# Kernel optimization log

Hardware: AMD Instinct MI355X
Metric: run time of the kernel (lower is better)

The kernel has to match this reference:

```python
import jax, jax.numpy as jnp
import numpy as np
import math

N = 20000          # nodes (residues)
E = 640000         # edges
CS = 384           # c_s
CZ = 128           # c_z
CH = 16            # c_hidden
H = 8              # no_heads
PQK = 8            # no_qk_points == no_v_points (forced equal, see notes)
FS = 128           # scalar channels in feat_irreps
PIN = 16           # vector channels in feat_irreps
HC = H * CH        # 128
HPQ = H * PQK * 3  # 192
CZ4 = CZ // 4      # 32
OUT_IN = HC + 3 * H + H + H * CZ4  # 416 actual concat width
INF = 100000.0
EPS = 1e-8


def setup_inputs() -> dict:
    key = jax.random.key(0)
    ks = jax.random.split(key, 16)
    w = lambda k, i, o: (jax.random.normal(k, (i, o), jnp.float32) / np.float32(np.sqrt(i)))
    frame_s = jax.random.normal(ks[0], (N, CS), jnp.float32)
    tfn_t = jax.random.normal(ks[1], (N, FS + 3 * PIN), jnp.float32)
    z = jax.random.normal(ks[2], (E, CZ), jnp.float32)
    edge_index = jax.random.randint(ks[3], (2, E), 0, N)
    mask = jnp.ones((N,), jnp.float32)
    # Rigid transforms: proper-ish rotations via QR, translations
    rot, _ = jnp.linalg.qr(jax.random.normal(ks[4], (N, 3, 3), jnp.float32))
    trans = jax.random.normal(ks[5], (N, 3), jnp.float32)
    return {
        "frame_s": frame_s, "tfn_t": tfn_t, "z": z,
        "edge_index": edge_index, "mask": mask,
        "rot": rot, "trans": trans,
        "Wq": w(ks[6], CS, HC), "bq": jnp.zeros((HC,), jnp.float32),
        "Wk_s": w(ks[7], FS, HC), "Wk_v": w(ks[8], PIN, PQK),
        "Wqp": w(ks[9], CS, HPQ), "bqp": jnp.zeros((HPQ,), jnp.float32),
        "Wb": w(ks[10], CZ, H), "bb": jnp.zeros((H,), jnp.float32),
        "Wdz": w(ks[11], CZ, CZ4), "bdz": jnp.zeros((CZ4,), jnp.float32),
        # ipa_point_weights_init_: softplus(hw) == 1  =>  hw = log(e - 1)
        "head_weights": jnp.full((H,), np.float32(np.log(np.e - 1.0))),
        "Wout": w(ks[12], OUT_IN, CS), "bout": jnp.zeros((CS,), jnp.float32),
    }


def _segment_softmax(a, seg, n):
    # pyg-style numerically stable segment softmax over edges grouped by seg
    m = jax.ops.segment_max(a, seg, num_segments=n)
    m = jnp.where(jnp.isfinite(m), m, 0.0)
    e = jnp.exp(a - m[seg])
    s = jax.ops.segment_sum(e, seg, num_segments=n)
    return e / (s[seg] + 1e-16)


def _forward(frame_s, tfn_t, z, mask, rot, trans,
             Wq, bq, Wk_s, Wk_v, Wqp, bqp, Wb, bb, Wdz, bdz,
             head_weights, Wout, bout, edge_index):
    n = frame_s.shape[0]
    src = edge_index[1]
    dst = edge_index[0]

    # scalar queries: [N,H,C]
    q = (frame_s @ Wq + bq).reshape(n, H, CH)

    # o3.Linear (feat_irreps -> k_irreps): scalars mix scalars, vectors mix vectors.
    # NOTE: original code uses linear_k for BOTH k and v (faithful bug), so v==k.
    scal = tfn_t[:, :FS]
    vecs = tfn_t[:, FS:].reshape(n, PIN, 3)
    k_scal = scal @ Wk_s                                   # [N, HC]
    k_vec = jnp.einsum('npx,pq->nqx', vecs, Wk_v)          # [N, PQK, 3]
    k = k_scal.reshape(n, H, CH)
    v = k
    k_tail = k_vec.reshape(n, PQK * 3)                     # [N, 24]
    # torch: split([3]*PQK) then stack(dim=-1) -> [N,3,PQK], then view [N,H,-1,3]
    k_pts = jnp.stack(jnp.split(k_tail, PQK, axis=-1), axis=-1)  # [N,3,PQK]
    k_pts = k_pts.reshape(n, H, -1, 3)                     # [N,H,1,3]
    v_pts = k_pts

    # query points, rigid-transformed: [N,H,PQK,3]
    q_pts = frame_s @ Wqp + bqp                            # [N, 3*H*PQK]
    q_pts = jnp.stack(jnp.split(q_pts, 3, axis=-1), axis=-1)  # [N, H*PQK, 3]
    q_pts = jnp.einsum('nij,npj->npi', rot, q_pts) + trans[:, None, :]
    q_pts = q_pts.reshape(n, H, PQK, 3)

    # scalar attention logits [E,H]
    a = jnp.einsum('ehc,ehc->eh', q[src], k[dst])
    a = a * np.float32(math.sqrt(1.0 / (3 * CH)))
    b = z @ Wb + bb                                        # [E,H]
    a = a + np.float32(math.sqrt(1.0 / 3)) * b

    # point attention: disp [E,H,PQK,3] (k_pts broadcasts over points)
    disp = q_pts[src] - k_pts[dst]
    pt_att = jnp.sum(disp * disp, axis=-1)                 # [E,H,PQK]
    hw = jax.nn.softplus(head_weights) * np.float32(math.sqrt(1.0 / (3 * (PQK * 9.0 / 2))))
    pt_att = -0.5 * jnp.sum(pt_att * hw[None, :, None], axis=-1)  # [E,H]

    edge_mask = INF * (mask[dst] * mask[src] - 1.0)        # [E]
    a = a + pt_att + edge_mask[:, None]

    a = _segment_softmax(a, src, n)                        # [E,H]

    # scalar output
    o = jax.ops.segment_sum(a[..., None] * v[dst], src, num_segments=n)  # [N,H,C]
    o = o.reshape(n, HC)

    # point output
    o_pt = jax.ops.segment_sum(a[:, :, None, None] * v_pts[dst], src, num_segments=n)  # [N,H,1,3]
    o_pt = jnp.einsum('nji,nhpj->nhpi', rot, o_pt - trans[:, None, None, :])  # invert_apply
    o_pt_norm = jnp.sqrt(jnp.sum(o_pt * o_pt, axis=-1) + EPS).reshape(n, H)
    o_pt = o_pt.reshape(n, -1, 3)                          # [N,H,3]

    # pair output
    pair_z = z @ Wdz + bdz                                 # [E,CZ4]
    o_pair = jax.ops.segment_sum(a[..., None] * pair_z[:, None, :], src, num_segments=n)  # [N,H,CZ4]
    o_pair = o_pair.reshape(n, H * CZ4)

    feats = jnp.concatenate(
        [o, o_pt[..., 0], o_pt[..., 1], o_pt[..., 2], o_pt_norm, o_pair], axis=-1)  # [N,416]
    return feats @ Wout + bout                             # [N, CS]


def reference(frame_s, tfn_t, z, edge_index, mask, rot, trans,
              Wq, bq, Wk_s, Wk_v, Wqp, bqp, Wb, bb, Wdz, bdz,
              head_weights, Wout, bout):
    return _forward(frame_s, tfn_t, z, mask, rot, trans,
                    Wq, bq, Wk_s, Wk_v, Wqp, bqp, Wb, bb, Wdz, bdz,
                    head_weights, Wout, bout, edge_index)
```

## Files before the change

### kernel.cpp

```cpp
#include <hip/hip_runtime.h>
#include <math.h>

typedef __attribute__((ext_vector_type(8))) short short8;
typedef __attribute__((ext_vector_type(4))) float f32x4;

static __device__ inline unsigned short f2bf(float f) {
    union { float f; unsigned u; } v; v.f = f;
    unsigned r = v.u + 0x7FFF + ((v.u >> 16) & 1);
    return (unsigned short)(r >> 16);
}

template<int WJ>
__device__ __forceinline__ void gemm_body(
    unsigned short* __restrict__ As, unsigned short* __restrict__ Bs,
    const float* __restrict__ A, int lda,
    const float* __restrict__ BT, int ldb,
    const float* __restrict__ bias,
    float* __restrict__ C, int ldc,
    int M, int N, int K, int bx, int by)
{
    constexpr int GBN = WJ * 32;
    const int t = threadIdx.x;
    const int wid = t >> 6, lane = t & 63;
    const int wm = (wid & 1) * 64;
    const int wn = (wid >> 1) * (WJ * 16);
    const int row16 = lane & 15, quad = lane >> 4;
    const int bm = bx * 128;
    const int bn = by * GBN;

    f32x4 acc[4][WJ];
    #pragma unroll
    for (int i = 0; i < 4; ++i)
        #pragma unroll
        for (int j = 0; j < WJ; ++j)
            #pragma unroll
            for (int r = 0; r < 4; ++r) acc[i][j][r] = 0.f;

    const int ktiles = (K + 63) >> 6;
    for (int kt = 0; kt < ktiles; ++kt) {
        const int k0 = kt << 6;
        #pragma unroll
        for (int it = 0; it < 8; ++it) {
            int f = it * 256 + t;
            int row = f >> 4, kq = (f & 15) << 2;
            float4 av = make_float4(0.f, 0.f, 0.f, 0.f);
            if (bm + row < M && k0 + kq < K)
                av = *(const float4*)(A + (size_t)(bm + row) * lda + k0 + kq);
            ushort4 uv;
            uv.x = f2bf(av.x); uv.y = f2bf(av.y); uv.z = f2bf(av.z); uv.w = f2bf(av.w);
            *(ushort4*)(&As[row * 72 + kq]) = uv;
        }
        #pragma unroll
        for (int it = 0; it < WJ * 2; ++it) {
            int f = it * 256 + t;
            int row = f >> 4, kq = (f & 15) << 2;
            float4 bv = make_float4(0.f, 0.f, 0.f, 0.f);
            if (bn + row < N && k0 + kq < K)
                bv = *(const float4*)(BT + (size_t)(bn + row) * ldb + k0 + kq);
            ushort4 uv;
            uv.x = f2bf(bv.x); uv.y = f2bf(bv.y); uv.z = f2bf(bv.z); uv.w = f2bf(bv.w);
            *(ushort4*)(&Bs[row * 72 + kq]) = uv;
        }
        __syncthreads();

        #pragma unroll
        for (int ks = 0; ks < 64; ks += 32) {
            short8 af[4], bfv[WJ];
            #pragma unroll
            for (int i = 0; i < 4; ++i)
                af[i] = *(const short8*)(&As[(wm + i * 16 + row16) * 72 + ks + quad * 8]);
            #pragma unroll
            for (int j = 0; j < WJ; ++j)
                bfv[j] = *(const short8*)(&Bs[(wn + j * 16 + row16) * 72 + ks + quad * 8]);
            #pragma unroll
            for (int i = 0; i < 4; ++i)
                #pragma unroll
                for (int j = 0; j < WJ; ++j)
                    acc[i][j] = __builtin_amdgcn_mfma_f32_16x16x32_bf16(af[i], bfv[j], acc[i][j], 0, 0, 0);
        }
        __syncthreads();
    }

    #pragma unroll
    for (int i = 0; i < 4; ++i)
        #pragma unroll
        for (int j = 0; j < WJ; ++j) {
            int col = bn + wn + j * 16 + row16;
            if (col >= N) continue;
            float bv = bias ? bias[col] : 0.f;
            #pragma unroll
            for (int r = 0; r < 4; ++r) {
                int row = bm + wm + i * 16 + quad * 4 + r;
                if (row < M) C[(size_t)row * ldc + col] = acc[i][j][r] + bv;
            }
        }
}

template<int WJ>
__global__ __launch_bounds__(256) void gemm_mfma(
    const float* __restrict__ A, int lda,
    const float* __restrict__ BT, int ldb,
    const float* __restrict__ bias,
    float* __restrict__ C, int ldc,
    int M, int N, int K)
{
    __shared__ unsigned short As[128 * 72];
    __shared__ unsigned short Bs[WJ * 32 * 72];
    gemm_body<WJ>(As, Bs, A, lda, BT, ldb, bias, C, ldc, M, N, K, blockIdx.x, blockIdx.y);
}

__device__ __forceinline__ void bpair_body(
    const float* __restrict__ z, const float* __restrict__ wcatT,
    const float* __restrict__ bcat, float* __restrict__ bpair, int E,
    int bb, int nbb)
{
    const int lane = threadIdx.x & 63;
    const int wid = threadIdx.x >> 6;
    const int row16 = lane & 15, quad = lane >> 4;

    short8 bfv[3][4];
    float bj[3];
    #pragma unroll
    for (int j = 0; j < 3; ++j) {
        int col = j * 16 + row16;
        bool cv = col < 40;
        bj[j] = cv ? bcat[col] : 0.f;
        #pragma unroll
        for (int ks = 0; ks < 4; ++ks) {
            float4 w0 = make_float4(0.f, 0.f, 0.f, 0.f);
            float4 w1 = make_float4(0.f, 0.f, 0.f, 0.f);
            if (cv) {
                const float* wp = wcatT + (size_t)col * 128 + ks * 32 + quad * 8;
                w0 = *(const float4*)(wp);
                w1 = *(const float4*)(wp + 4);
            }
            short8 f;
            f[0] = (short)f2bf(w0.x); f[1] = (short)f2bf(w0.y);
            f[2] = (short)f2bf(w0.z); f[3] = (short)f2bf(w0.w);
            f[4] = (short)f2bf(w1.x); f[5] = (short)f2bf(w1.y);
            f[6] = (short)f2bf(w1.z); f[7] = (short)f2bf(w1.w);
            bfv[j][ks] = f;
        }
    }

    const int nstrips = (E + 31) >> 5;
    const int gw = bb * 4 + wid;
    const int nw = nbb * 4;
    for (int st = gw; st < nstrips; st += nw) {
        const int r0 = st * 32;
        short8 af[2][4];
        #pragma unroll
        for (int i = 0; i < 2; ++i) {
            int row = r0 + i * 16 + row16;
            bool rv = row < E;
            const float* zp = z + (size_t)row * 128 + quad * 8;
            #pragma unroll
            for (int ks = 0; ks < 4; ++ks) {
                float4 a0 = make_float4(0.f, 0.f, 0.f, 0.f);
                float4 a1 = make_float4(0.f, 0.f, 0.f, 0.f);
                if (rv) {
                    a0 = *(const float4*)(zp + ks * 32);
                    a1 = *(const float4*)(zp + ks * 32 + 4);
                }
                short8 f;
                f[0] = (short)f2bf(a0.x); f[1] = (short)f2bf(a0.y);
                f[2] = (short)f2bf(a0.z); f[3] = (short)f2bf(a0.w);
                f[4] = (short)f2bf(a1.x); f[5] = (short)f2bf(a1.y);
                f[6] = (short)f2bf(a1.z); f[7] = (short)f2bf(a1.w);
                af[i][ks] = f;
            }
        }

        f32x4 acc[2][3];
        #pragma unroll
        for (int i = 0; i < 2; ++i)
            #pragma unroll
            for (int j = 0; j < 3; ++j)
                #pragma unroll
                for (int r = 0; r < 4; ++r) acc[i][j][r] = 0.f;

        #pragma unroll
        for (int ks = 0; ks < 4; ++ks)
            #pragma unroll
            for (int i = 0; i < 2; ++i)
                #pragma unroll
                for (int j = 0; j < 3; ++j)
                    acc[i][j] = __builtin_amdgcn_mfma_f32_16x16x32_bf16(af[i][ks], bfv[j][ks], acc[i][j], 0, 0, 0);

        #pragma unroll
        for (int i = 0; i < 2; ++i)
            #pragma unroll
            for (int j = 0; j < 3; ++j) {
                int col = j * 16 + row16;
                if (col >= 40) continue;
                #pragma unroll
                for (int r = 0; r < 4; ++r) {
                    int row = r0 + i * 16 + quad * 4 + r;
                    if (row < E) bpair[(size_t)row * 40 + col] = acc[i][j][r] + bj[j];
                }
            }
    }
}

__global__ __launch_bounds__(256) void mega_kernel(
    const float* __restrict__ z, const float* __restrict__ wcatT,
    const float* __restrict__ bcat, float* __restrict__ bpair, int E,
    const float* __restrict__ frame_s, const float* __restrict__ wqqpT,
    const float* __restrict__ bqqp, float* __restrict__ qqp, int n,
    const float* __restrict__ tfn, const float* __restrict__ wksT,
    float* __restrict__ kbuf,
    const float* __restrict__ Wkv, float* __restrict__ kpts,
    const int* __restrict__ srcA, const int* __restrict__ dstA,
    int* __restrict__ cur, int2* __restrict__ einfo,
    int nb_bp, int nb_qqp_x, int nb_qqp, int nb_k, int nb_kpts)
{
    __shared__ unsigned short As[128 * 72];
    __shared__ unsigned short Bs[128 * 72];
    int b = blockIdx.x;
    if (b < nb_bp) {
        bpair_body(z, wcatT, bcat, bpair, E, b, nb_bp);
        return;
    }
    b -= nb_bp;
    if (b < nb_qqp) {
        gemm_body<4>(As, Bs, frame_s, 384, wqqpT, 384, bqqp, qqp, 320, n, 320, 384,
                     b % nb_qqp_x, b / nb_qqp_x);
        return;
    }
    b -= nb_qqp;
    if (b < nb_k) {
        gemm_body<4>(As, Bs, tfn, 176, wksT, 128, nullptr, kbuf, 128, n, 128, 128, b, 0);
        return;
    }
    b -= nb_k;
    if (b < nb_kpts) {
        int t = b * 256 + threadIdx.x;
        if (t < n * 24) {
            int node = t / 24, f = t % 24;
            int a = f >> 3;
            int bb2 = f & 7;
            const float* vr = tfn + (size_t)node * 176 + 128;
            float s = 0.f;
            #pragma unroll
            for (int p = 0; p < 16; ++p) s += vr[p * 3 + a] * Wkv[p * 8 + bb2];
            kpts[t] = s;
        }
        return;
    }
    b -= nb_kpts;
    {
        int e = b * 256 + threadIdx.x;
        if (e < E) {
            int s = srcA[e];
            int pos = atomicAdd(&cur[s], 1);
            einfo[pos] = make_int2(e, dstA[e]);
        }
    }
}

__global__ void prep_count_kernel(
    const float* __restrict__ Wq, const float* __restrict__ bq,
    const float* __restrict__ Wqp, const float* __restrict__ bqp,
    const float* __restrict__ Wb, const float* __restrict__ bb,
    const float* __restrict__ Wdz, const float* __restrict__ bdz,
    const float* __restrict__ Wks, const float* __restrict__ Wout,
    float* __restrict__ wqqpT, float* __restrict__ bqqp,
    float* __restrict__ wcatT, float* __restrict__ bcat,
    float* __restrict__ wksT, float* __restrict__ woutT,
    const int* __restrict__ srcA, int* __restrict__ cnt, int E, int nb_cnt)
{
    int b = blockIdx.x;
    if (b < nb_cnt) {
        int e = b * 256 + threadIdx.x;
        if (e < E) atomicAdd(&cnt[srcA[e]], 1);
        return;
    }
    b -= nb_cnt;
    const float SC_QK = 0.14433756729740643f;
    const float SC_B  = 0.5773502691896258f;
    int gid = b * 256 + threadIdx.x;
    int stride = (gridDim.x - nb_cnt) * 256;
    for (int i = gid; i < 320 * 384; i += stride) {
        int o = i / 384, c = i % 384;
        wqqpT[i] = (o < 128) ? Wq[c * 128 + o] * SC_QK : Wqp[c * 192 + (o - 128)];
    }
    for (int i = gid; i < 320; i += stride) bqqp[i] = (i < 128) ? bq[i] * SC_QK : bqp[i - 128];
    for (int i = gid; i < 40 * 128; i += stride) {
        int o = i >> 7, c = i & 127;
        wcatT[i] = (o < 8) ? Wb[c * 8 + o] * SC_B : Wdz[c * 32 + (o - 8)];
    }
    for (int i = gid; i < 40; i += stride) bcat[i] = (i < 8) ? bb[i] * SC_B : bdz[i - 8];
    for (int i = gid; i < 128 * 128; i += stride) {
        int o = i >> 7, c = i & 127;
        wksT[i] = Wks[c * 128 + o];
    }
    for (int i = gid; i < 384 * 416; i += stride) {
        int o = i / 416, c = i % 416;
        woutT[i] = Wout[c * 384 + o];
    }
}

__global__ void scan_kernel(const int* __restrict__ cnt, int* __restrict__ off,
                            int* __restrict__ cur, int n)
{
    __shared__ int sums[1024];
    int t = threadIdx.x;
    int chunk = (n + 1023) >> 10;
    int begin = t * chunk;
    int local = 0;
    for (int j = 0; j < chunk; ++j) {
        int i = begin + j;
        if (i < n) local += cnt[i];
    }
    sums[t] = local;
    __syncthreads();
    for (int d = 1; d < 1024; d <<= 1) {
        int x = sums[t];
        int y = (t >= d) ? sums[t - d] : 0;
        __syncthreads();
        sums[t] = x + y;
        __syncthreads();
    }
    int run = sums[t] - local;
    for (int j = 0; j < chunk; ++j) {
        int i = begin + j;
        if (i < n) {
            off[i] = run;
            cur[i] = run;
            run += cnt[i];
        }
    }
}

__global__ __launch_bounds__(256) void attn_kernel(
    const int* __restrict__ off, const int* __restrict__ cnt,
    const int2* __restrict__ einfo,
    const float* __restrict__ qqp, const float* __restrict__ kbuf,
    const float* __restrict__ kpts,
    const float* __restrict__ bpair, const float* __restrict__ mask,
    const float* __restrict__ hwin,
    const float* __restrict__ rot, const float* __restrict__ trans,
    float* __restrict__ feats, int n)
{
    int wave = threadIdx.x >> 6;
    int lane = threadIdx.x & 63;
    int s = blockIdx.x * 4 + wave;
    if (s >= n) return;
    int es = lane >> 3;
    int h  = lane & 7;

    float qh[16];
    {
        const float* qp = qqp + (size_t)s * 320 + h * 16;
        #pragma unroll
        for (int c = 0; c < 16; ++c) qh[c] = qp[c];
    }
    const float* Rp = rot + (size_t)s * 9;
    const float* Tp = trans + (size_t)s * 3;
    float R0 = Rp[0], R1 = Rp[1], R2 = Rp[2];
    float R3 = Rp[3], R4 = Rp[4], R5 = Rp[5];
    float R6 = Rp[6], R7 = Rp[7], R8 = Rp[8];
    float T0 = Tp[0], T1 = Tp[1], T2 = Tp[2];
    float qpt[24];
    {
        const float* qr = qqp + (size_t)s * 320 + 128 + h * 8;
        #pragma unroll
        for (int p2 = 0; p2 < 8; ++p2) {
            float c0 = qr[p2], c1 = qr[64 + p2], c2 = qr[128 + p2];
            qpt[p2 * 3 + 0] = R0 * c0 + R1 * c1 + R2 * c2 + T0;
            qpt[p2 * 3 + 1] = R3 * c0 + R4 * c1 + R5 * c2 + T1;
            qpt[p2 * 3 + 2] = R6 * c0 + R7 * c1 + R8 * c2 + T2;
        }
    }
    float hwv = log1pf(__expf(hwin[h])) * 0.04811252243246882f;
    float mask_s = mask[s];
    int myoff = off[s], mycnt = cnt[s];

    float ssum = 0.f;
    float oacc[16];
    #pragma unroll
    for (int c = 0; c < 16; ++c) oacc[c] = 0.f;
    float optacc[3] = {0.f, 0.f, 0.f};
    float opacc[8][4];
    #pragma unroll
    for (int j = 0; j < 8; ++j)
        #pragma unroll
        for (int c = 0; c < 4; ++c) opacc[j][c] = 0.f;

    int nb = (mycnt + 7) >> 3;
    int2 ed = make_int2(0, 0);
    if (nb > 0) {
        int pos0 = (es < mycnt) ? myoff + es : (mycnt > 0 ? myoff : 0);
        ed = einfo[pos0];
    }
    for (int b = 0; b < nb; ++b) {
        int idx = b * 8 + es;
        bool valid = idx < mycnt;
        int e = ed.x, d = ed.y;
        int2 ned = ed;
        if (b + 1 < nb) {
            int nidx = idx + 8;
            int npos = (nidx < mycnt) ? myoff + nidx : myoff;
            ned = einfo[npos];
        }

        const float* kr = kbuf + (size_t)d * 128 + h * 16;
        float4 ka = *(const float4*)(kr + 0);
        float4 kb = *(const float4*)(kr + 4);
        float4 kc = *(const float4*)(kr + 8);
        float4 kd = *(const float4*)(kr + 12);

        const float* kp = kpts + (size_t)d * 24 + h * 3;
        float kp0 = kp[0], kp1 = kp[1], kp2 = kp[2];

        const float* bp = bpair + (size_t)e * 40;
        float bh = bp[h];
        float4 pair4 = *(const float4*)(bp + 8 + h * 4);

        float qk = qh[0] * ka.x + qh[1] * ka.y + qh[2] * ka.z + qh[3] * ka.w
                 + qh[4] * kb.x + qh[5] * kb.y + qh[6] * kb.z + qh[7] * kb.w
                 + qh[8] * kc.x + qh[9] * kc.y + qh[10] * kc.z + qh[11] * kc.w
                 + qh[12] * kd.x + qh[13] * kd.y + qh[14] * kd.z + qh[15] * kd.w;

        float pt = 0.f;
        #pragma unroll
        for (int pp = 0; pp < 8; ++pp) {
            float d0 = qpt[pp * 3 + 0] - kp0;
            float d1 = qpt[pp * 3 + 1] - kp1;
            float d2 = qpt[pp * 3 + 2] - kp2;
            pt += d0 * d0 + d1 * d1 + d2 * d2;
        }

        float md = mask[d];
        float logit = qk + bh - hwv * pt + 100000.0f * (mask_s * md - 1.0f);
        float w = valid ? __expf(logit) : 0.f;

        ssum += w;
        oacc[0] += w * ka.x; oacc[1] += w * ka.y; oacc[2] += w * ka.z; oacc[3] += w * ka.w;
        oacc[4] += w * kb.x; oacc[5] += w * kb.y; oacc[6] += w * kb.z; oacc[7] += w * kb.w;
        oacc[8] += w * kc.x; oacc[9] += w * kc.y; oacc[10] += w * kc.z; oacc[11] += w * kc.w;
        oacc[12] += w * kd.x; oacc[13] += w * kd.y; oacc[14] += w * kd.z; oacc[15] += w * kd.w;
        optacc[0] += w * kp0;
        optacc[1] += w * kp1;
        optacc[2] += w * kp2;

        #pragma unroll
        for (int jh = 0; jh < 8; ++jh) {
            float wj = __shfl(w, (es << 3) + jh);
            opacc[jh][0] += wj * pair4.x;
            opacc[jh][1] += wj * pair4.y;
            opacc[jh][2] += wj * pair4.z;
            opacc[jh][3] += wj * pair4.w;
        }
        ed = ned;
    }

    #pragma unroll
    for (int delta = 8; delta <= 32; delta <<= 1) {
        ssum += __shfl_xor(ssum, delta);
        #pragma unroll
        for (int c = 0; c < 16; ++c) oacc[c] += __shfl_xor(oacc[c], delta);
        #pragma unroll
        for (int i = 0; i < 3; ++i) optacc[i] += __shfl_xor(optacc[i], delta);
        #pragma unroll
        for (int j = 0; j < 8; ++j)
            #pragma unroll
            for (int c = 0; c < 4; ++c) opacc[j][c] += __shfl_xor(opacc[j][c], delta);
    }

    float invj[8];
    #pragma unroll
    for (int jh = 0; jh < 8; ++jh)
        invj[jh] = 1.f / (__shfl(ssum, jh) + 1e-16f);

    if (es == 0) {
        float inv = 1.f / (ssum + 1e-16f);
        float* f = feats + (size_t)s * 416;
        #pragma unroll
        for (int c = 0; c < 16; c += 4) {
            float4 v = make_float4(oacc[c] * inv, oacc[c + 1] * inv, oacc[c + 2] * inv, oacc[c + 3] * inv);
            *(float4*)(&f[h * 16 + c]) = v;
        }
        float v0 = optacc[0] * inv - T0;
        float v1 = optacc[1] * inv - T1;
        float v2 = optacc[2] * inv - T2;
        float r0 = R0 * v0 + R3 * v1 + R6 * v2;
        float r1 = R1 * v0 + R4 * v1 + R7 * v2;
        float r2 = R2 * v0 + R5 * v1 + R8 * v2;
        f[128 + h] = r0;
        f[136 + h] = r1;
        f[144 + h] = r2;
        f[152 + h] = sqrtf(r0 * r0 + r1 * r1 + r2 * r2 + 1e-8f);
        #pragma unroll
        for (int jh = 0; jh < 8; ++jh) {
            float4 v = make_float4(opacc[jh][0] * invj[jh], opacc[jh][1] * invj[jh],
                                   opacc[jh][2] * invj[jh], opacc[jh][3] * invj[jh]);
            *(float4*)(&f[160 + jh * 32 + h * 4]) = v;
        }
    }
}

extern "C" void kernel_launch(void* const* d_in, const int* in_sizes, int n_in,
                              void* d_out, int out_size, void* d_ws, size_t ws_size,
                              hipStream_t stream)
{
    const float* frame_s = (const float*)d_in[0];
    const float* tfn     = (const float*)d_in[1];
    const float* z       = (const float*)d_in[2];
    const int*   ei      = (const int*)d_in[3];
    const float* mask    = (const float*)d_in[4];
    const float* rot     = (const float*)d_in[5];
    const float* trans   = (const float*)d_in[6];
    const float* Wq      = (const float*)d_in[7];
    const float* bq      = (const float*)d_in[8];
    const float* Wks     = (const float*)d_in[9];
    const float* Wkv     = (const float*)d_in[10];
    const float* Wqp     = (const float*)d_in[11];
    const float* bqp     = (const float*)d_in[12];
    const float* Wb      = (const float*)d_in[13];
    const float* bb      = (const float*)d_in[14];
    const float* Wdz     = (const float*)d_in[15];
    const float* bdz     = (const float*)d_in[16];
    const float* hw      = (const float*)d_in[17];
    const float* Wout    = (const float*)d_in[18];
    const float* bout    = (const float*)d_in[19];
    float* out = (float*)d_out;

    int n = in_sizes[0] / 384;
    int E = in_sizes[3] / 2;
    const int* dstA = ei;
    const int* srcA = ei + E;

    float* ws = (float*)d_ws;
    size_t p = 0;
    auto alloc = [&](size_t elems) -> float* {
        float* r = ws + p;
        p += (elems + 15) & ~((size_t)15);
        return r;
    };
    float* qqpbuf = alloc((size_t)n * 320);
    float* kbuf   = alloc((size_t)n * 128);
    float* kpts   = alloc((size_t)n * 24);
    float* feats  = alloc((size_t)n * 416);
    float* bpair  = alloc((size_t)E * 40);
    float* wqqpT  = alloc(320 * 384);
    float* bqqp   = alloc(320);
    float* wcatT  = alloc(40 * 128);
    float* bcat   = alloc(64);
    float* wksT   = alloc(128 * 128);
    float* woutT  = alloc(384 * 416);
    int*  cnt   = (int*)alloc((size_t)n);
    int*  off   = (int*)alloc((size_t)n);
    int*  cur   = (int*)alloc((size_t)n);
    int2* einfo = (int2*)alloc((size_t)E * 2);

    hipMemsetAsync(cnt, 0, (size_t)n * sizeof(int), stream);

    int nb_cnt = (E + 255) / 256;
    prep_count_kernel<<<nb_cnt + 512, 256, 0, stream>>>(
        Wq, bq, Wqp, bqp, Wb, bb, Wdz, bdz, Wks, Wout,
        wqqpT, bqqp, wcatT, bcat, wksT, woutT,
        srcA, cnt, E, nb_cnt);

    scan_kernel<<<1, 1024, 0, stream>>>(cnt, off, cur, n);

    int nb_bp    = 2048;
    int nb_qqp_x = (n + 127) / 128;
    int nb_qqp   = nb_qqp_x * 3;
    int nb_k     = (n + 127) / 128;
    int nb_kpts  = (n * 24 + 255) / 256;
    int nb_fill  = (E + 255) / 256;
    int nb_total = nb_bp + nb_qqp + nb_k + nb_kpts + nb_fill;
    mega_kernel<<<nb_total, 256, 0, stream>>>(
        z, wcatT, bcat, bpair, E,
        frame_s, wqqpT, bqqp, qqpbuf, n,
        tfn, wksT, kbuf,
        Wkv, kpts,
        srcA, dstA, cur, einfo,
        nb_bp, nb_qqp_x, nb_qqp, nb_k, nb_kpts);

    attn_kernel<<<(n + 3) / 4, 256, 0, stream>>>(off, cnt, einfo,
                                                 qqpbuf, kbuf, kpts, bpair, mask, hw,
                                                 rot, trans, feats, n);

    {
        dim3 g((n + 127) / 128, 3);
        gemm_mfma<4><<<g, 256, 0, stream>>>(feats, 416, woutT, 416, bout, out, 384, n, 384, 416);
    }
    (void)n_in; (void)out_size; (void)ws_size;
}
```

Baseline: 815.6 us.

## Use K=32 GEMM tiles, reorder mega-kernel blocks, widen output GEMM tile

Adds a gemm32_body variant that stages 32-wide K tiles into smaller shared buffers, and uses it for the qqp and k projections inside the mega kernel. Shared memory per block shrinks, which may allow more resident blocks. The bpair blocks move to the end of the grid and their count goes from 2048 to 4096, so the short GEMM and fill blocks are dispatched first. The output GEMM switches to a 6-wide N tile with 2 column blocks instead of 3. The cost is more K-loop iterations and barriers in the projections, and higher register pressure in the output GEMM.

```diff
diff --git a/kernel.cpp b/kernel.cpp
--- a/kernel.cpp
+++ b/kernel.cpp
@@ -107,6 +107,89 @@
     __shared__ unsigned short As[128 * 72];
     __shared__ unsigned short Bs[WJ * 32 * 72];
     gemm_body<WJ>(As, Bs, A, lda, BT, ldb, bias, C, ldc, M, N, K, blockIdx.x, blockIdx.y);
+}
+
+template<int WJ>
+__device__ __forceinline__ void gemm32_body(
+    unsigned short* __restrict__ As, unsigned short* __restrict__ Bs,
+    const float* __restrict__ A, int lda,
+    const float* __restrict__ BT, int ldb,
+    const float* __restrict__ bias,
+    float* __restrict__ C, int ldc,
+    int M, int N, int K, int bx, int by)
+{
+    constexpr int GBN = WJ * 32;
+    const int t = threadIdx.x;
+    const int wid = t >> 6, lane = t & 63;
+    const int wm = (wid & 1) * 64;
+    const int wn = (wid >> 1) * (WJ * 16);
+    const int row16 = lane & 15, quad = lane >> 4;
+    const int bm = bx * 128;
+    const int bn = by * GBN;
+
+    f32x4 acc[4][WJ];
+    #pragma unroll
+    for (int i = 0; i < 4; ++i)
+        #pragma unroll
+        for (int j = 0; j < WJ; ++j)
+            #pragma unroll
+            for (int r = 0; r < 4; ++r) acc[i][j][r] = 0.f;
+
+    const int ktiles = (K + 31) >> 5;
+    for (int kt = 0; kt < ktiles; ++kt) {
+        const int k0 = kt << 5;
+        #pragma unroll
+        for (int it = 0; it < 4; ++it) {
+            int f = it * 256 + t;
+            int row = f >> 3, kq = (f & 7) << 2;
+            float4 av = make_float4(0.f, 0.f, 0.f, 0.f);
+            if (bm + row < M && k0 + kq < K)
+                av = *(const float4*)(A + (size_t)(bm + row) * lda + k0 + kq);
+            ushort4 uv;
+            uv.x = f2bf(av.x); uv.y = f2bf(av.y); uv.z = f2bf(av.z); uv.w = f2bf(av.w);
+            *(ushort4*)(&As[row * 40 + kq]) = uv;
+        }
+        #pragma unroll
+        for (int it = 0; it < WJ; ++it) {
+            int f = it * 256 + t;
+            int row = f >> 3, kq = (f & 7) << 2;
+            float4 bv = make_float4(0.f, 0.f, 0.f, 0.f);
+            if (bn + row < N && k0 + kq < K)
+                bv = *(const float4*)(BT + (size_t)(bn + row) * ldb + k0 + kq);
+            ushort4 uv;
+            uv.x = f2bf(bv.x); uv.y = f2bf(bv.y); uv.z = f2bf(bv.z); uv.w = f2bf(bv.w);
+            *(ushort4*)(&Bs[row * 40 + kq]) = uv;
+        }
+        __syncthreads();
+
+        short8 af[4], bfv[WJ];
+        #pragma unroll
+        for (int i = 0; i < 4; ++i)
+            af[i] = *(const short8*)(&As[(wm + i * 16 + row16) * 40 + quad * 8]);
+        #pragma unroll
+        for (int j = 0; j < WJ; ++j)
+            bfv[j] = *(const short8*)(&Bs[(wn + j * 16 + row16) * 40 + quad * 8]);
+        #pragma unroll
+        for (int i = 0; i < 4; ++i)
+            #pragma unroll
+            for (int j = 0; j < WJ; ++j)
+                acc[i][j] = __builtin_amdgcn_mfma_f32_16x16x32_bf16(af[i], bfv[j], acc[i][j], 0, 0, 0);
+        __syncthreads();
+    }
+
+    #pragma unroll
+    for (int i = 0; i < 4; ++i)
+        #pragma unroll
+        for (int j = 0; j < WJ; ++j) {
+            int col = bn + wn + j * 16 + row16;
+            if (col >= N) continue;
+            float bv = bias ? bias[col] : 0.f;
+            #pragma unroll
+            for (int r = 0; r < 4; ++r) {
+                int row = bm + wm + i * 16 + quad * 4 + r;
+                if (row < M) C[(size_t)row * ldc + col] = acc[i][j][r] + bv;
+            }
+        }
 }
 
 __device__ __forceinline__ void bpair_body(
@@ -212,24 +295,19 @@
     const float* __restrict__ Wkv, float* __restrict__ kpts,
     const int* __restrict__ srcA, const int* __restrict__ dstA,
     int* __restrict__ cur, int2* __restrict__ einfo,
-    int nb_bp, int nb_qqp_x, int nb_qqp, int nb_k, int nb_kpts)
-{
-    __shared__ unsigned short As[128 * 72];
-    __shared__ unsigned short Bs[128 * 72];
+    int nb_qqp_x, int nb_qqp, int nb_k, int nb_kpts, int nb_fill, int nb_bp)
+{
+    __shared__ unsigned short As[128 * 40];
+    __shared__ unsigned short Bs[128 * 40];
     int b = blockIdx.x;
-    if (b < nb_bp) {
-        bpair_body(z, wcatT, bcat, bpair, E, b, nb_bp);
-        return;
-    }
-    b -= nb_bp;
     if (b < nb_qqp) {
-        gemm_body<4>(As, Bs, frame_s, 384, wqqpT, 384, bqqp, qqp, 320, n, 320, 384,
-                     b % nb_qqp_x, b / nb_qqp_x);
+        gemm32_body<4>(As, Bs, frame_s, 384, wqqpT, 384, bqqp, qqp, 320, n, 320, 384,
+                       b % nb_qqp_x, b / nb_qqp_x);
         return;
     }
     b -= nb_qqp;
     if (b < nb_k) {
-        gemm_body<4>(As, Bs, tfn, 176, wksT, 128, nullptr, kbuf, 128, n, 128, 128, b, 0);
+        gemm32_body<4>(As, Bs, tfn, 176, wksT, 128, nullptr, kbuf, 128, n, 128, 128, b, 0);
         return;
     }
     b -= nb_k;
@@ -248,14 +326,17 @@
         return;
     }
     b -= nb_kpts;
-    {
+    if (b < nb_fill) {
         int e = b * 256 + threadIdx.x;
         if (e < E) {
             int s = srcA[e];
             int pos = atomicAdd(&cur[s], 1);
             einfo[pos] = make_int2(e, dstA[e]);
         }
-    }
+        return;
+    }
+    b -= nb_fill;
+    bpair_body(z, wcatT, bcat, bpair, E, b, nb_bp);
 }
 
 __global__ void prep_count_kernel(
@@ -564,28 +645,28 @@
 
     scan_kernel<<<1, 1024, 0, stream>>>(cnt, off, cur, n);
 
-    int nb_bp    = 2048;
     int nb_qqp_x = (n + 127) / 128;
     int nb_qqp   = nb_qqp_x * 3;
     int nb_k     = (n + 127) / 128;
     int nb_kpts  = (n * 24 + 255) / 256;
     int nb_fill  = (E + 255) / 256;
-    int nb_total = nb_bp + nb_qqp + nb_k + nb_kpts + nb_fill;
+    int nb_bp    = 4096;
+    int nb_total = nb_qqp + nb_k + nb_kpts + nb_fill + nb_bp;
     mega_kernel<<<nb_total, 256, 0, stream>>>(
         z, wcatT, bcat, bpair, E,
         frame_s, wqqpT, bqqp, qqpbuf, n,
         tfn, wksT, kbuf,
         Wkv, kpts,
         srcA, dstA, cur, einfo,
-        nb_bp, nb_qqp_x, nb_qqp, nb_k, nb_kpts);
+        nb_qqp_x, nb_qqp, nb_k, nb_kpts, nb_fill, nb_bp);
 
     attn_kernel<<<(n + 3) / 4, 256, 0, stream>>>(off, cnt, einfo,
                                                  qqpbuf, kbuf, kpts, bpair, mask, hw,
                                                  rot, trans, feats, n);
 
     {
-        dim3 g((n + 127) / 128, 3);
-        gemm_mfma<4><<<g, 256, 0, stream>>>(feats, 416, woutT, 416, bout, out, 384, n, 384, 416);
+        dim3 g((n + 127) / 128, 2);
+        gemm_mfma<6><<<g, 256, 0, stream>>>(feats, 416, woutT, 416, bout, out, 384, n, 384, 416);
     }
     (void)n_in; (void)out_size; (void)ws_size;
 }
```

Result: slower. 841.6 us (+3.2%).
